# Kernel optimization log

Measured on AMD Instinct MI355X. Metric: run time of the kernel, lower is better.

## Reference

```python
import jax, jax.numpy as jnp
import numpy as np

N, E = 20000, 640000
LATENT, HID, OUT, HEADS = 512, 256, 128, 2
NEG_SLOPE = 0.2


def setup_inputs() -> dict:
    key = jax.random.key(0)
    ks = jax.random.split(key, 12)
    s = 0.02
    return {
        "z": jax.random.normal(ks[0], (N, LATENT), dtype=jnp.float32),
        "edge_index": jax.random.randint(ks[1], (2, E), 0, N, dtype=jnp.int64),
        "W1": jax.random.normal(ks[2], (LATENT, HID), dtype=jnp.float32) * s,
        "b1": jnp.zeros((HID,), dtype=jnp.float32),
        "W2": jax.random.normal(ks[3], (HID, HID * HEADS), dtype=jnp.float32) * s,
        "b2": jnp.zeros((HID * HEADS,), dtype=jnp.float32),
        "Wg": jax.random.normal(ks[4], (HID * HEADS, HEADS * OUT), dtype=jnp.float32) * s,
        "att_src": jax.random.normal(ks[5], (HEADS, OUT), dtype=jnp.float32) * s,
        "att_dst": jax.random.normal(ks[6], (HEADS, OUT), dtype=jnp.float32) * s,
        "bias_g": jnp.zeros((HEADS * OUT,), dtype=jnp.float32),
        "W3": jax.random.normal(ks[7], (OUT * HEADS, 512), dtype=jnp.float32) * s,
        "b3": jnp.zeros((512,), dtype=jnp.float32),
    }


def _gat_conv(x, edge_index, Wg, att_src, att_dst, bias_g):
    n = x.shape[0]
    # add self loops (PyG GATConv default add_self_loops=True)
    loops = jnp.tile(jnp.arange(n, dtype=edge_index.dtype)[None, :], (2, 1))
    ei = jnp.concatenate([edge_index, loops], axis=1)
    src, dst = ei[0], ei[1]
    xp = (x @ Wg).reshape(n, HEADS, OUT)          # [N,H,C]
    a_src = jnp.einsum('nhc,hc->nh', xp, att_src)  # [N,H]
    a_dst = jnp.einsum('nhc,hc->nh', xp, att_dst)
    alpha = jax.nn.leaky_relu(a_src[src] + a_dst[dst], NEG_SLOPE)  # [E+N,H]
    amax = jax.ops.segment_max(alpha, dst, num_segments=n)
    alpha = jnp.exp(alpha - amax[dst])
    denom = jax.ops.segment_sum(alpha, dst, num_segments=n)
    alpha = alpha / jnp.maximum(denom[dst], 1e-16)
    msg = xp[src] * alpha[:, :, None]              # [E+N,H,C]
    out = jax.ops.segment_sum(msg, dst, num_segments=n)  # [N,H,C]
    return out.reshape(n, HEADS * OUT) + bias_g


def reference(z, edge_index, W1, b1, W2, b2, Wg, att_src, att_dst, bias_g, W3, b3):
    x = jax.nn.relu(z @ W1 + b1)
    x = jax.nn.relu(x @ W2 + b2)
    x = _gat_conv(x, edge_index, Wg, att_src, att_dst, bias_g)
    return x @ W3 + b3
```

## Files before the change

### kernel.cpp

```cpp
#include <hip/hip_runtime.h>
#include <hip/hip_bf16.h>
#include <float.h>

#define N_NODES 20000
#define LATENT  512
#define HID     256
#define OUT_C   128
#define HEADS   2
#define HC      256
#define NEG_SLOPE 0.2f

typedef _Float16 half8 __attribute__((ext_vector_type(8)));
typedef __attribute__((ext_vector_type(4))) float f32x4;

__device__ __forceinline__ ushort f2h(float v) {
    _Float16 h = (_Float16)v;
    return *(ushort*)&h;
}
__device__ __forceinline__ float h2f(ushort u) {
    _Float16 h = *(_Float16*)&u;
    return (float)h;
}

__device__ __forceinline__ void gl_lds16(const ushort* g, ushort* l) {
    __builtin_amdgcn_global_load_lds(
        (const __attribute__((address_space(1))) unsigned int*)g,
        (__attribute__((address_space(3))) unsigned int*)l, 16, 0, 0);
}

template<int BN>
__global__ __launch_bounds__(256, 4) void gemm_f16(
    const ushort* __restrict__ A, const ushort* __restrict__ BT,
    const float* __restrict__ bias,
    float* __restrict__ Cf, ushort* __restrict__ Ch,
    int M, int N, int K, int relu)
{
    static_assert(BN == 64, "vmcnt immediates assume 3 DMAs/chunk");
    constexpr int NI  = BN / 32;
    constexpr int BUF = 4096 + BN * 32;
    __shared__ ushort lds[3 * BUF];

    const int t = threadIdx.x;
    const int l = t & 63;
    const int w = t >> 6;
    const int wm = (w >> 1) * 64;
    const int wn = (w & 1) * (BN / 2);
    const int lm = l & 15;
    const int q  = l >> 4;
    const int q4 = q * 4;

    const int row0 = blockIdx.x * 128;
    const int col0 = blockIdx.y * BN;

    const int jr0 = w * 16 + (l >> 2);
    const int gsh = (((l & 3) ^ ((l >> 4) & 3)) << 3);
    const ushort* gA0 = A + (size_t)(row0 + jr0) * K + gsh;
    const ushort* gA1 = gA0 + (size_t)64 * K;
    const ushort* gB0 = BT + (size_t)(col0 + jr0) * K + gsh;
    const int dA0 = w * 512, dA1 = (4 + w) * 512;
    const int dB0 = 4096 + w * 512;

    const int csw = ((q ^ ((lm >> 2) & 3)) << 3);

    const f32x4 zf = {0.f, 0.f, 0.f, 0.f};
    f32x4 acc[4][NI];
    #pragma unroll
    for (int i = 0; i < 4; ++i)
        #pragma unroll
        for (int j = 0; j < NI; ++j) acc[i][j] = zf;

    const int NC = K >> 5;

    auto issue = [&](int c) {
        ushort* B = lds + (size_t)(c % 3) * BUF;
        const int kk = c * 32;
        gl_lds16(gA0 + kk, B + dA0);
        gl_lds16(gA1 + kk, B + dA1);
        gl_lds16(gB0 + kk, B + dB0);
    };

    auto compute = [&](int c) {
        const ushort* B = lds + (size_t)(c % 3) * BUF;
        half8 bf[NI];
        #pragma unroll
        for (int ni = 0; ni < NI; ++ni) {
            const int boff = (wn + ni * 16 + lm) * 32 + csw;
            bf[ni] = *(const half8*)&B[4096 + boff];
        }
        #pragma unroll
        for (int mi = 0; mi < 4; ++mi) {
            const int aoff = (wm + mi * 16 + lm) * 32 + csw;
            half8 af = *(const half8*)&B[aoff];
            #pragma unroll
            for (int ni = 0; ni < NI; ++ni)
                acc[mi][ni] = __builtin_amdgcn_mfma_f32_16x16x32_f16(
                    af, bf[ni], acc[mi][ni], 0, 0, 0);
        }
    };

    issue(0); issue(1);
    for (int c = 0; c < NC; ++c) {
        __builtin_amdgcn_sched_barrier(0);
        if (c + 1 < NC) asm volatile("s_waitcnt vmcnt(3)" ::: "memory");
        else            asm volatile("s_waitcnt vmcnt(0)" ::: "memory");
        __builtin_amdgcn_s_barrier();
        __builtin_amdgcn_sched_barrier(0);
        if (c + 2 < NC) issue(c + 2);
        compute(c);
    }

    #pragma unroll
    for (int mi = 0; mi < 4; ++mi) {
        #pragma unroll
        for (int ni = 0; ni < NI; ++ni) {
            const int col = col0 + wn + ni * 16 + lm;
            const float bv = bias ? bias[col] : 0.f;
            #pragma unroll
            for (int r = 0; r < 4; ++r) {
                const int row = row0 + wm + mi * 16 + q4 + r;
                if (row >= M) continue;
                float v = acc[mi][ni][r] + bv;
                if (relu) v = fmaxf(v, 0.f);
                const size_t idx = (size_t)row * N + col;
                if (Cf) Cf[idx] = v;
                if (Ch) Ch[idx] = f2h(v);
            }
        }
    }
}

#define CVT_BLOCKS 10000
#define TR_BLOCKS  2048
__global__ __launch_bounds__(256) void prologue_kernel(
    const float* __restrict__ z, ushort* __restrict__ z_f16,
    int* deg, int* cursor, int n,
    const float* __restrict__ W1, const float* __restrict__ W2,
    const float* __restrict__ Wg, const float* __restrict__ W3,
    ushort* __restrict__ T1, ushort* __restrict__ T2,
    ushort* __restrict__ Tg, ushort* __restrict__ T3)
{
    const int b = blockIdx.x;
    if (b < CVT_BLOCKS) {
        int i = b * 256 + threadIdx.x;
        if (i < n) { deg[i] = 0; cursor[i] = 0; }
        float4 v = ((const float4*)z)[i];
        ((ushort4*)z_f16)[i] = make_ushort4(f2h(v.x), f2h(v.y), f2h(v.z), f2h(v.w));
    } else {
        int idx = (b - CVT_BLOCKS) * 256 + threadIdx.x;
        int which = idx >> 17, i = idx & 131071;
        const float* W; ushort* T; int K, N;
        if (which == 0)      { W = W1; T = T1; K = 512; N = 256; }
        else if (which == 1) { W = W2; T = T2; K = 256; N = 512; }
        else if (which == 2) { W = Wg; T = Tg; K = 512; N = 256; }
        else                 { W = W3; T = T3; K = 256; N = 512; }
        int k = i / N, nn = i - k * N;
        T[(size_t)nn * K + k] = f2h(W[i]);
    }
}

__global__ __launch_bounds__(256) void hist_kernel(
    const int* __restrict__ dst, int* deg, int E_real, int ET)
{
    int e = blockIdx.x * blockDim.x + threadIdx.x;
    if (e >= ET) return;
    int d = (e < E_real) ? dst[e] : (e - E_real);
    atomicAdd(&deg[d], 1);
}

__global__ __launch_bounds__(1024) void att_scan_kernel(
    const ushort* __restrict__ xp, const float* __restrict__ att_src,
    const float* __restrict__ att_dst,
    float* __restrict__ a_src, float* __restrict__ a_dst,
    const int* __restrict__ deg, int* __restrict__ rowptr, int n)
{
    __shared__ int part[1024];
    if (blockIdx.x < 1250) {
        int node = blockIdx.x * 16 + (threadIdx.x >> 6);
        int lane = threadIdx.x & 63;
        int h = lane >> 5, lh = lane & 31;
        int c = h * OUT_C + lh * 4;
        const ushort4 v = *(const ushort4*)(xp + (size_t)node * HC + c);
        const float4 as = *(const float4*)(att_src + c);
        const float4 ad = *(const float4*)(att_dst + c);
        float x0 = h2f(v.x), x1 = h2f(v.y), x2 = h2f(v.z), x3 = h2f(v.w);
        float s1 = x0 * as.x + x1 * as.y + x2 * as.z + x3 * as.w;
        float s2 = x0 * ad.x + x1 * ad.y + x2 * ad.z + x3 * ad.w;
        #pragma unroll
        for (int off = 16; off > 0; off >>= 1) {
            s1 += __shfl_xor(s1, off);
            s2 += __shfl_xor(s2, off);
        }
        if (lh == 0) { a_src[2 * node + h] = s1; a_dst[2 * node + h] = s2; }
    } else {
        const int t = threadIdx.x;
        const int chunk = (n + 1023) / 1024;
        const int lo = t * chunk;
        const int hi = min(lo + chunk, n);
        int s = 0;
        for (int i = lo; i < hi; ++i) s += deg[i];
        part[t] = s;
        __syncthreads();
        #pragma unroll
        for (int off = 1; off < 1024; off <<= 1) {
            int add = (t >= off) ? part[t - off] : 0;
            __syncthreads();
            part[t] += add;
            __syncthreads();
        }
        int run = part[t] - s;
        for (int i = lo; i < hi; ++i) { rowptr[i] = run; run += deg[i]; }
        if (t == 1023) rowptr[n] = part[1023];
    }
}

__global__ __launch_bounds__(256) void scatter_kernel(
    const int* __restrict__ src, const int* __restrict__ dst,
    const int* __restrict__ rowptr, int* cursor,
    int* __restrict__ sorted_src, int E_real, int ET)
{
    int e = blockIdx.x * blockDim.x + threadIdx.x;
    if (e >= ET) return;
    int s, d;
    if (e < E_real) { s = src[e]; d = dst[e]; }
    else            { s = e - E_real; d = s; }
    int pos = rowptr[d] + atomicAdd(&cursor[d], 1);
    sorted_src[pos] = s;
}

__global__ __launch_bounds__(256) void gat_aggregate(
    const int* __restrict__ rowptr, const int* __restrict__ sorted_src,
    const float* __restrict__ a_src, const float* __restrict__ a_dst,
    const ushort* __restrict__ xp, const float* __restrict__ bias_g,
    ushort* __restrict__ xg, int n)
{
    const int d = blockIdx.x * 4 + (threadIdx.x >> 6);
    if (d >= n) return;
    const int lane = threadIdx.x & 63;
    const int hsel = lane & 32;
    const int start = rowptr[d], end = rowptr[d + 1];

    const float ad0 = a_dst[2 * d + 0];
    const float ad1 = a_dst[2 * d + 1];

    float4 acc = make_float4(0.f, 0.f, 0.f, 0.f);
    float denom = 0.f;

    for (int e0 = start; e0 < end; e0 += 32) {
        const int cnt = min(32, end - e0);
        const int idx = lane & 31;
        float wsel = 0.f; int off = 0;
        if (idx < cnt) {
            int s = sorted_src[e0 + idx];
            float v0 = a_src[2 * s + 0] + ad0;
            float v1 = a_src[2 * s + 1] + ad1;
            v0 = (v0 > 0.f) ? v0 : NEG_SLOPE * v0;
            v1 = (v1 > 0.f) ? v1 : NEG_SLOPE * v1;
            wsel = (lane < 32) ? __expf(v0) : __expf(v1);
            off = s * HC;
        }
        int j = 0;
        for (; j + 8 <= cnt; j += 8) {
            float w_[8]; int o_[8];
            #pragma unroll
            for (int u = 0; u < 8; ++u) {
                w_[u] = __shfl(wsel, (j + u) + hsel);
                o_[u] = __shfl(off, j + u);
            }
            ushort4 v_[8];
            #pragma unroll
            for (int u = 0; u < 8; ++u)
                v_[u] = *(const ushort4*)(xp + o_[u] + 4 * lane);
            #pragma unroll
            for (int u = 0; u < 8; ++u) {
                denom += w_[u];
                acc.x += w_[u] * h2f(v_[u].x);
                acc.y += w_[u] * h2f(v_[u].y);
                acc.z += w_[u] * h2f(v_[u].z);
                acc.w += w_[u] * h2f(v_[u].w);
            }
        }
        for (; j < cnt; ++j) {
            const float w = __shfl(wsel, j + hsel);
            const int   o = __shfl(off, j);
            const ushort4 v = *(const ushort4*)(xp + o + 4 * lane);
            denom += w;
            acc.x += w * h2f(v.x); acc.y += w * h2f(v.y);
            acc.z += w * h2f(v.z); acc.w += w * h2f(v.w);
        }
    }

    const float inv = 1.f / fmaxf(denom, 1e-16f);
    const int c = 4 * lane;
    const float4 bg = *(const float4*)(bias_g + c);
    const size_t base = ((size_t)d * HC + c) >> 2;
    ((ushort4*)xg)[base] = make_ushort4(
        f2h(acc.x * inv + bg.x), f2h(acc.y * inv + bg.y),
        f2h(acc.z * inv + bg.z), f2h(acc.w * inv + bg.w));
}

extern "C" void kernel_launch(void* const* d_in, const int* in_sizes, int n_in,
                              void* d_out, int out_size, void* d_ws, size_t ws_size,
                              hipStream_t stream)
{
    const float* z       = (const float*)d_in[0];
    const int*   ei      = (const int*)d_in[1];
    const float* W1      = (const float*)d_in[2];
    const float* b1      = (const float*)d_in[3];
    const float* W2      = (const float*)d_in[4];
    const float* b2      = (const float*)d_in[5];
    const float* Wg      = (const float*)d_in[6];
    const float* att_src = (const float*)d_in[7];
    const float* att_dst = (const float*)d_in[8];
    const float* bias_g  = (const float*)d_in[9];
    const float* W3      = (const float*)d_in[10];
    const float* b3      = (const float*)d_in[11];
    float* out = (float*)d_out;

    const int n = N_NODES;
    const int E_real = in_sizes[1] / 2;
    const int ET = E_real + n;
    const int* src = ei;
    const int* dst = ei + E_real;

    char* p = (char*)d_ws;
    auto alloc = [&](size_t bytes) {
        char* r = p;
        p += (bytes + 63) & ~(size_t)63;
        return r;
    };
    const int np = n + 128;
    ushort* z_f16  = (ushort*)alloc((size_t)np * LATENT * 2);
    ushort* x1_f16 = (ushort*)alloc((size_t)np * HID * 2);
    ushort* xp_f16 = (ushort*)alloc((size_t)n * HC * 2);
    ushort* W1T = (ushort*)alloc((size_t)LATENT * HID * 2);
    ushort* W2T = (ushort*)alloc((size_t)HID * 512 * 2);
    ushort* WgT = (ushort*)alloc((size_t)512 * HC * 2);
    ushort* W3T = (ushort*)alloc((size_t)HC * 512 * 2);
    float* a_src = (float*)alloc((size_t)2 * n * 4);
    float* a_dst = (float*)alloc((size_t)2 * n * 4);
    int* deg        = (int*)alloc((size_t)n * 4);
    int* rowptr     = (int*)alloc(((size_t)n + 1) * 4);
    int* cursor     = (int*)alloc((size_t)n * 4);
    int* sorted_src = (int*)alloc((size_t)ET * 4);
    ushort* x2_f16 = z_f16;
    ushort* xg_f16 = x1_f16;

    const int gm128 = (n + 127) / 128;

    prologue_kernel<<<CVT_BLOCKS + TR_BLOCKS, 256, 0, stream>>>(
        z, z_f16, deg, cursor, n, W1, W2, Wg, W3, W1T, W2T, WgT, W3T);
    hist_kernel<<<(ET + 255) / 256, 256, 0, stream>>>(dst, deg, E_real, ET);

    gemm_f16<64><<<dim3(gm128, HID / 64), 256, 0, stream>>>(
        z_f16, W1T, b1, nullptr, x1_f16, n, HID, LATENT, 1);
    gemm_f16<64><<<dim3(gm128, 512 / 64), 256, 0, stream>>>(
        x1_f16, W2T, b2, nullptr, x2_f16, n, 512, HID, 1);
    gemm_f16<64><<<dim3(gm128, HC / 64), 256, 0, stream>>>(
        x2_f16, WgT, nullptr, nullptr, xp_f16, n, HC, 512, 0);

    att_scan_kernel<<<1251, 1024, 0, stream>>>(
        xp_f16, att_src, att_dst, a_src, a_dst, deg, rowptr, n);
    scatter_kernel<<<(ET + 255) / 256, 256, 0, stream>>>(
        src, dst, rowptr, cursor, sorted_src, E_real, ET);
    gat_aggregate<<<(n + 3) / 4, 256, 0, stream>>>(
        rowptr, sorted_src, a_src, a_dst, xp_f16, bias_g, xg_f16, n);

    gemm_f16<64><<<dim3(gm128, 512 / 64), 256, 0, stream>>>(
        xg_f16, W3T, b3, out, nullptr, n, 512, HC, 0);
}
```

Measured before the change: 335.4 us.

## Store GAT projections in FP8 and fuse attention logits into projection GEMM epilogue

The projection GEMM now writes xp in FP8 e4m3, using the hardware conversion builtins when they exist and a software fallback otherwise. Its epilogue also computes the per-node attention logits with shuffles and atomicAdds into buffers zeroed in the prologue, so the separate attention kernel is gone and the scan is split into its own single-block kernel. The graph CSR build is moved ahead of the GEMMs. The goal is to halve the bytes of the random gather in aggregation and drop one xp pass, at the cost of FP8 precision loss and atomic contention on the logits.

```diff
diff --git a/kernel.cpp b/kernel.cpp
--- a/kernel.cpp
+++ b/kernel.cpp
@@ -12,6 +12,7 @@
 
 typedef _Float16 half8 __attribute__((ext_vector_type(8)));
 typedef __attribute__((ext_vector_type(4))) float f32x4;
+typedef __attribute__((ext_vector_type(2))) float f32x2;
 
 __device__ __forceinline__ ushort f2h(float v) {
     _Float16 h = (_Float16)v;
@@ -20,6 +21,26 @@
 __device__ __forceinline__ float h2f(ushort u) {
     _Float16 h = *(_Float16*)&u;
     return (float)h;
+}
+
+#if __has_builtin(__builtin_amdgcn_cvt_pk_fp8_f32) && __has_builtin(__builtin_amdgcn_cvt_pk_f32_fp8)
+#define FP8_HW 1
+#else
+#define FP8_HW 0
+#endif
+
+__device__ __forceinline__ uint f32_to_e4m3(float v) {
+#if FP8_HW
+    return (uint)(__builtin_amdgcn_cvt_pk_fp8_f32(v, v, 0, false) & 0xff);
+#else
+    _Float16 hf = (_Float16)(v * 0.00390625f);
+    uint hb = *(ushort*)&hf;
+    uint s = (hb >> 8) & 0x80;
+    uint mag = hb & 0x7fff;
+    mag = (mag + 0x3f + ((mag >> 7) & 1)) >> 7;
+    if (mag > 0x7e) mag = 0x7e;
+    return s | mag;
+#endif
 }
 
 __device__ __forceinline__ void gl_lds16(const ushort* g, ushort* l) {
@@ -33,6 +54,9 @@
     const ushort* __restrict__ A, const ushort* __restrict__ BT,
     const float* __restrict__ bias,
     float* __restrict__ Cf, ushort* __restrict__ Ch,
+    unsigned char* __restrict__ C8,
+    const float* __restrict__ attS, const float* __restrict__ attD,
+    float* __restrict__ aS, float* __restrict__ aD,
     int M, int N, int K, int relu)
 {
     static_assert(BN == 64, "vmcnt immediates assume 3 DMAs/chunk");
@@ -124,6 +148,40 @@
                 const size_t idx = (size_t)row * N + col;
                 if (Cf) Cf[idx] = v;
                 if (Ch) Ch[idx] = f2h(v);
+                if (C8) C8[idx] = (unsigned char)f32_to_e4m3(v);
+            }
+        }
+    }
+
+    if (aS) {
+        const int h = (col0 >= OUT_C) ? 1 : 0;
+        float asv[NI], adv[NI];
+        #pragma unroll
+        for (int ni = 0; ni < NI; ++ni) {
+            const int c = col0 + wn + ni * 16 + lm;
+            asv[ni] = attS[c];
+            adv[ni] = attD[c];
+        }
+        #pragma unroll
+        for (int mi = 0; mi < 4; ++mi) {
+            #pragma unroll
+            for (int r = 0; r < 4; ++r) {
+                const int row = row0 + wm + mi * 16 + q4 + r;
+                float ps = 0.f, pd = 0.f;
+                #pragma unroll
+                for (int ni = 0; ni < NI; ++ni) {
+                    ps += acc[mi][ni][r] * asv[ni];
+                    pd += acc[mi][ni][r] * adv[ni];
+                }
+                #pragma unroll
+                for (int off = 8; off > 0; off >>= 1) {
+                    ps += __shfl_xor(ps, off);
+                    pd += __shfl_xor(pd, off);
+                }
+                if (lm == 0 && row < M) {
+                    atomicAdd(&aS[2 * row + h], ps);
+                    atomicAdd(&aD[2 * row + h], pd);
+                }
             }
         }
     }
@@ -133,7 +191,7 @@
 #define TR_BLOCKS  2048
 __global__ __launch_bounds__(256) void prologue_kernel(
     const float* __restrict__ z, ushort* __restrict__ z_f16,
-    int* deg, int* cursor, int n,
+    int* deg, int* cursor, float* aS, float* aD, int n,
     const float* __restrict__ W1, const float* __restrict__ W2,
     const float* __restrict__ Wg, const float* __restrict__ W3,
     ushort* __restrict__ T1, ushort* __restrict__ T2,
@@ -142,7 +200,11 @@
     const int b = blockIdx.x;
     if (b < CVT_BLOCKS) {
         int i = b * 256 + threadIdx.x;
-        if (i < n) { deg[i] = 0; cursor[i] = 0; }
+        if (i < n) {
+            deg[i] = 0; cursor[i] = 0;
+            ((float2*)aS)[i] = make_float2(0.f, 0.f);
+            ((float2*)aD)[i] = make_float2(0.f, 0.f);
+        }
         float4 v = ((const float4*)z)[i];
         ((ushort4*)z_f16)[i] = make_ushort4(f2h(v.x), f2h(v.y), f2h(v.z), f2h(v.w));
     } else {
@@ -167,50 +229,28 @@
     atomicAdd(&deg[d], 1);
 }
 
-__global__ __launch_bounds__(1024) void att_scan_kernel(
-    const ushort* __restrict__ xp, const float* __restrict__ att_src,
-    const float* __restrict__ att_dst,
-    float* __restrict__ a_src, float* __restrict__ a_dst,
+__global__ __launch_bounds__(1024) void scan_kernel(
     const int* __restrict__ deg, int* __restrict__ rowptr, int n)
 {
     __shared__ int part[1024];
-    if (blockIdx.x < 1250) {
-        int node = blockIdx.x * 16 + (threadIdx.x >> 6);
-        int lane = threadIdx.x & 63;
-        int h = lane >> 5, lh = lane & 31;
-        int c = h * OUT_C + lh * 4;
-        const ushort4 v = *(const ushort4*)(xp + (size_t)node * HC + c);
-        const float4 as = *(const float4*)(att_src + c);
-        const float4 ad = *(const float4*)(att_dst + c);
-        float x0 = h2f(v.x), x1 = h2f(v.y), x2 = h2f(v.z), x3 = h2f(v.w);
-        float s1 = x0 * as.x + x1 * as.y + x2 * as.z + x3 * as.w;
-        float s2 = x0 * ad.x + x1 * ad.y + x2 * ad.z + x3 * ad.w;
-        #pragma unroll
-        for (int off = 16; off > 0; off >>= 1) {
-            s1 += __shfl_xor(s1, off);
-            s2 += __shfl_xor(s2, off);
-        }
-        if (lh == 0) { a_src[2 * node + h] = s1; a_dst[2 * node + h] = s2; }
-    } else {
-        const int t = threadIdx.x;
-        const int chunk = (n + 1023) / 1024;
-        const int lo = t * chunk;
-        const int hi = min(lo + chunk, n);
-        int s = 0;
-        for (int i = lo; i < hi; ++i) s += deg[i];
-        part[t] = s;
+    const int t = threadIdx.x;
+    const int chunk = (n + 1023) / 1024;
+    const int lo = t * chunk;
+    const int hi = min(lo + chunk, n);
+    int s = 0;
+    for (int i = lo; i < hi; ++i) s += deg[i];
+    part[t] = s;
+    __syncthreads();
+    #pragma unroll
+    for (int off = 1; off < 1024; off <<= 1) {
+        int add = (t >= off) ? part[t - off] : 0;
         __syncthreads();
-        #pragma unroll
-        for (int off = 1; off < 1024; off <<= 1) {
-            int add = (t >= off) ? part[t - off] : 0;
-            __syncthreads();
-            part[t] += add;
-            __syncthreads();
-        }
-        int run = part[t] - s;
-        for (int i = lo; i < hi; ++i) { rowptr[i] = run; run += deg[i]; }
-        if (t == 1023) rowptr[n] = part[1023];
-    }
+        part[t] += add;
+        __syncthreads();
+    }
+    int run = part[t] - s;
+    for (int i = lo; i < hi; ++i) { rowptr[i] = run; run += deg[i]; }
+    if (t == 1023) rowptr[n] = part[1023];
 }
 
 __global__ __launch_bounds__(256) void scatter_kernel(
@@ -230,7 +270,7 @@
 __global__ __launch_bounds__(256) void gat_aggregate(
     const int* __restrict__ rowptr, const int* __restrict__ sorted_src,
     const float* __restrict__ a_src, const float* __restrict__ a_dst,
-    const ushort* __restrict__ xp, const float* __restrict__ bias_g,
+    const unsigned char* __restrict__ xp8, const float* __restrict__ bias_g,
     ushort* __restrict__ xg, int n)
 {
     const int d = blockIdx.x * 4 + (threadIdx.x >> 6);
@@ -266,26 +306,45 @@
                 w_[u] = __shfl(wsel, (j + u) + hsel);
                 o_[u] = __shfl(off, j + u);
             }
-            ushort4 v_[8];
+            uint v_[8];
             #pragma unroll
             for (int u = 0; u < 8; ++u)
-                v_[u] = *(const ushort4*)(xp + o_[u] + 4 * lane);
+                v_[u] = *(const uint*)(xp8 + o_[u] + 4 * lane);
             #pragma unroll
             for (int u = 0; u < 8; ++u) {
                 denom += w_[u];
-                acc.x += w_[u] * h2f(v_[u].x);
-                acc.y += w_[u] * h2f(v_[u].y);
-                acc.z += w_[u] * h2f(v_[u].z);
-                acc.w += w_[u] * h2f(v_[u].w);
+#if FP8_HW
+                f32x2 lo = __builtin_amdgcn_cvt_pk_f32_fp8((int)v_[u], false);
+                f32x2 hi = __builtin_amdgcn_cvt_pk_f32_fp8((int)v_[u], true);
+                acc.x += w_[u] * lo.x; acc.y += w_[u] * lo.y;
+                acc.z += w_[u] * hi.x; acc.w += w_[u] * hi.y;
+#else
+                const float wu = w_[u] * 256.0f;
+                const uint b = v_[u];
+                acc.x += wu * h2f(((b & 0x80u) << 8) | ((b & 0x7fu) << 7));
+                acc.y += wu * h2f((((b >> 8) & 0x80u) << 8) | (((b >> 8) & 0x7fu) << 7));
+                acc.z += wu * h2f((((b >> 16) & 0x80u) << 8) | (((b >> 16) & 0x7fu) << 7));
+                acc.w += wu * h2f((((b >> 24) & 0x80u) << 8) | (((b >> 24) & 0x7fu) << 7));
+#endif
             }
         }
         for (; j < cnt; ++j) {
             const float w = __shfl(wsel, j + hsel);
             const int   o = __shfl(off, j);
-            const ushort4 v = *(const ushort4*)(xp + o + 4 * lane);
+            const uint  b = *(const uint*)(xp8 + o + 4 * lane);
             denom += w;
-            acc.x += w * h2f(v.x); acc.y += w * h2f(v.y);
-            acc.z += w * h2f(v.z); acc.w += w * h2f(v.w);
+#if FP8_HW
+            f32x2 lo = __builtin_amdgcn_cvt_pk_f32_fp8((int)b, false);
+            f32x2 hi = __builtin_amdgcn_cvt_pk_f32_fp8((int)b, true);
+            acc.x += w * lo.x; acc.y += w * lo.y;
+            acc.z += w * hi.x; acc.w += w * hi.y;
+#else
+            const float wu = w * 256.0f;
+            acc.x += wu * h2f(((b & 0x80u) << 8) | ((b & 0x7fu) << 7));
+            acc.y += wu * h2f((((b >> 8) & 0x80u) << 8) | (((b >> 8) & 0x7fu) << 7));
+            acc.z += wu * h2f((((b >> 16) & 0x80u) << 8) | (((b >> 16) & 0x7fu) << 7));
+            acc.w += wu * h2f((((b >> 24) & 0x80u) << 8) | (((b >> 24) & 0x7fu) << 7));
+#endif
         }
     }
 
@@ -331,7 +390,7 @@
     const int np = n + 128;
     ushort* z_f16  = (ushort*)alloc((size_t)np * LATENT * 2);
     ushort* x1_f16 = (ushort*)alloc((size_t)np * HID * 2);
-    ushort* xp_f16 = (ushort*)alloc((size_t)n * HC * 2);
+    unsigned char* xp8 = (unsigned char*)alloc((size_t)n * HC);
     ushort* W1T = (ushort*)alloc((size_t)LATENT * HID * 2);
     ushort* W2T = (ushort*)alloc((size_t)HID * 512 * 2);
     ushort* WgT = (ushort*)alloc((size_t)512 * HC * 2);
@@ -348,23 +407,27 @@
     const int gm128 = (n + 127) / 128;
 
     prologue_kernel<<<CVT_BLOCKS + TR_BLOCKS, 256, 0, stream>>>(
-        z, z_f16, deg, cursor, n, W1, W2, Wg, W3, W1T, W2T, WgT, W3T);
+        z, z_f16, deg, cursor, a_src, a_dst, n,
+        W1, W2, Wg, W3, W1T, W2T, WgT, W3T);
     hist_kernel<<<(ET + 255) / 256, 256, 0, stream>>>(dst, deg, E_real, ET);
-
-    gemm_f16<64><<<dim3(gm128, HID / 64), 256, 0, stream>>>(
-        z_f16, W1T, b1, nullptr, x1_f16, n, HID, LATENT, 1);
-    gemm_f16<64><<<dim3(gm128, 512 / 64), 256, 0, stream>>>(
-        x1_f16, W2T, b2, nullptr, x2_f16, n, 512, HID, 1);
-    gemm_f16<64><<<dim3(gm128, HC / 64), 256, 0, stream>>>(
-        x2_f16, WgT, nullptr, nullptr, xp_f16, n, HC, 512, 0);
-
-    att_scan_kernel<<<1251, 1024, 0, stream>>>(
-        xp_f16, att_src, att_dst, a_src, a_dst, deg, rowptr, n);
+    scan_kernel<<<1, 1024, 0, stream>>>(deg, rowptr, n);
     scatter_kernel<<<(ET + 255) / 256, 256, 0, stream>>>(
         src, dst, rowptr, cursor, sorted_src, E_real, ET);
+
+    gemm_f16<64><<<dim3(gm128, HID / 64), 256, 0, stream>>>(
+        z_f16, W1T, b1, nullptr, x1_f16, nullptr,
+        nullptr, nullptr, nullptr, nullptr, n, HID, LATENT, 1);
+    gemm_f16<64><<<dim3(gm128, 512 / 64), 256, 0, stream>>>(
+        x1_f16, W2T, b2, nullptr, x2_f16, nullptr,
+        nullptr, nullptr, nullptr, nullptr, n, 512, HID, 1);
+    gemm_f16<64><<<dim3(gm128, HC / 64), 256, 0, stream>>>(
+        x2_f16, WgT, nullptr, nullptr, nullptr, xp8,
+        att_src, att_dst, a_src, a_dst, n, HC, 512, 0);
+
     gat_aggregate<<<(n + 3) / 4, 256, 0, stream>>>(
-        rowptr, sorted_src, a_src, a_dst, xp_f16, bias_g, xg_f16, n);
+        rowptr, sorted_src, a_src, a_dst, xp8, bias_g, xg_f16, n);
 
     gemm_f16<64><<<dim3(gm128, 512 / 64), 256, 0, stream>>>(
-        xg_f16, W3T, b3, out, nullptr, n, 512, HC, 0);
-}
+        xg_f16, W3T, b3, out, nullptr, nullptr,
+        nullptr, nullptr, nullptr, nullptr, n, 512, HC, 0);
+}
```

Result: faster. 328.7 us (-2.0%).
